# Optimization experiments

Hardware: AMD Instinct MI355X
Metric: run time of the kernel (lower is better)

## Reference

```python
import jax, jax.numpy as jnp
import numpy as np

P = 2          # SamplesLoss p=2
BLUR = 0.05    # eps_final = BLUR**P = 0.0025
SCALING = 0.8  # annealing factor per iteration (on the blur scale)


def _cost(x, y):
    # geomloss cost for p=2: |x - y|^2 / 2, shape (N, M)
    x2 = jnp.sum(x * x, axis=-1)
    y2 = jnp.sum(y * y, axis=-1)
    return 0.5 * (x2[:, None] + y2[None, :] - 2.0 * (x @ y.T))


def _softmin(eps, C, h):
    # -eps * log sum_j exp(h_j - C_ij / eps); h already contains log-weights
    return -eps * jax.nn.logsumexp(h[None, :] - C / eps, axis=1)


def _eps_schedule(x, y):
    # geomloss scaling_parameters / epsilon_schedule with diameter from bounding box
    xn, yn = np.asarray(x), np.asarray(y)
    mins = np.minimum(xn.min(0), yn.min(0))
    maxs = np.maximum(xn.max(0), yn.max(0))
    diameter = float(np.linalg.norm(maxs - mins))
    eps_list = ([diameter ** P]
                + [float(np.exp(e)) for e in np.arange(P * np.log(diameter), P * np.log(BLUR), P * np.log(SCALING))]
                + [BLUR ** P])
    return eps_list


def _sinkhorn_divergence(x, y, eps_list):
    # Debiased Sinkhorn divergence S_eps(x, y), geomloss sinkhorn_tensorized
    N, M = x.shape[0], y.shape[0]
    sg = jax.lax.stop_gradient
    C_xy, C_yx = _cost(x, y), _cost(y, x)
    C_xx, C_yy = _cost(x, sg(x)), _cost(y, sg(y))  # geomloss detaches 2nd arg
    # The annealing loop runs with autograd disabled in geomloss:
    Cxy_, Cyx_, Cxx_, Cyy_ = sg(C_xy), sg(C_yx), sg(C_xx), sg(C_yy)
    a_log = jnp.full((N,), -np.log(N), dtype=x.dtype)  # log uniform weights
    b_log = jnp.full((M,), -np.log(M), dtype=y.dtype)
    e0 = eps_list[0]
    f_aa = _softmin(e0, Cxx_, a_log)
    g_bb = _softmin(e0, Cyy_, b_log)
    g_ab = _softmin(e0, Cyx_, a_log)
    f_ba = _softmin(e0, Cxy_, b_log)
    for eps in eps_list:  # fixed schedule, not a data-dim loop
        ft_ba = _softmin(eps, Cxy_, b_log + g_ab / eps)
        gt_ab = _softmin(eps, Cyx_, a_log + f_ba / eps)
        ft_aa = _softmin(eps, Cxx_, a_log + f_aa / eps)
        gt_bb = _softmin(eps, Cyy_, b_log + g_bb / eps)
        f_ba, g_ab = 0.5 * (f_ba + ft_ba), 0.5 * (g_ab + gt_ab)
        f_aa, g_bb = 0.5 * (f_aa + ft_aa), 0.5 * (g_bb + gt_bb)
    # Final extrapolation step (the only one geomloss differentiates through):
    eps = eps_list[-1]
    f_ba, g_ab = (_softmin(eps, C_xy, sg(b_log + g_ab / eps)),
                  _softmin(eps, C_yx, sg(a_log + f_ba / eps)))
    f_aa = _softmin(eps, C_xx, sg(a_log + f_aa / eps))
    g_bb = _softmin(eps, C_yy, sg(b_log + g_bb / eps))
    # scal with uniform weights == mean
    return jnp.mean(f_ba - f_aa) + jnp.mean(g_ab - g_bb)


def setup_inputs() -> dict:
    key = jax.random.key(0)
    kx, kt = jax.random.split(key)
    x = jax.random.normal(kx, (4096, 64), dtype=jnp.float32)
    target = jax.random.normal(kt, (4096, 64), dtype=jnp.float32)
    return {"x": x, "target": target}


def reference(x, target):
    eps_list = _eps_schedule(x, target)  # concrete schedule from data diameter
    return _sinkhorn_divergence(x, target, eps_list)
```

## Files before the change

### kernel.cpp

```cpp
#include <hip/hip_runtime.h>
#include <math.h>

#define NPTS 4096
#define DIM  64
#define MAX_ITERS 36

#define ALOG (-8.317766166719343f)
#define L2E  (1.4426950408889634f)
#define LN2  (0.6931471805599453f)

#if __has_builtin(__builtin_amdgcn_exp2f)
#define EXP2F(x) __builtin_amdgcn_exp2f(x)
#else
#define EXP2F(x) exp2f(x)
#endif
#if __has_builtin(__builtin_amdgcn_logf)
#define LOG2F(x) __builtin_amdgcn_logf(x)
#else
#define LOG2F(x) log2f(x)
#endif

typedef _Float16 half8 __attribute__((ext_vector_type(8)));

__global__ void minmax_part_kernel(const float* __restrict__ x,
                                   const float* __restrict__ y,
                                   float* __restrict__ partmn,
                                   float* __restrict__ partmx) {
    int t = threadIdx.x;
    int bid = blockIdx.x;
    int g0 = bid * 256 + t;
    const int total = NPTS * DIM;
    float mn = INFINITY, mx = -INFINITY;
    for (int g = g0; g < total; g += 128 * 256) {
        float v = x[g]; mn = fminf(mn, v); mx = fmaxf(mx, v);
        float w = y[g]; mn = fminf(mn, w); mx = fmaxf(mx, w);
    }
    __shared__ float smn[256], smx[256];
    smn[t] = mn; smx[t] = mx;
    __syncthreads();
    if (t < 64) {
        for (int q = 1; q < 4; q++) {
            mn = fminf(mn, smn[t + 64 * q]);
            mx = fmaxf(mx, smx[t + 64 * q]);
        }
        partmn[bid * 64 + t] = mn;
        partmx[bid * 64 + t] = mx;
    }
}

__global__ void schedule_kernel(const float* __restrict__ partmn,
                                const float* __restrict__ partmx,
                                int* __restrict__ hdr,
                                float* __restrict__ sched) {
    int d = threadIdx.x;
    float mn = INFINITY, mx = -INFINITY;
    for (int b = 0; b < 128; b++) {
        mn = fminf(mn, partmn[b * 64 + d]);
        mx = fmaxf(mx, partmx[b * 64 + d]);
    }
    float range = mx - mn;
    __shared__ float r2[64];
    r2[d] = range * range;
    __syncthreads();
    if (d == 0) {
        float ss = 0.f;
        for (int k = 0; k < 64; k++) ss += r2[k];
        float diam_f = sqrtf(ss);
        double diam = (double)diam_f;
        double start = 2.0 * log(diam);
        double stop  = 2.0 * log(0.05);
        double step  = 2.0 * log(0.8);
        int n_ar = (int)ceil((stop - start) / step);
        if (n_ar < 0) n_ar = 0;
        int n_eps = n_ar + 2;
        if (n_eps > 64) n_eps = 64;
        sched[0] = (float)(diam * diam);
        for (int k = 0; k < n_ar && (1 + k) < 63; k++)
            sched[1 + k] = (float)exp(start + step * (double)k);
        sched[n_eps - 1] = 0.0025f;
        for (int k = n_eps; k < 64; k++) sched[k] = 0.0025f;
        hdr[0] = n_eps;
    }
}

__global__ void sqnorm_kernel(const float* __restrict__ X, float* __restrict__ out) {
    int wave = (blockIdx.x * blockDim.x + threadIdx.x) >> 6;
    int lane = threadIdx.x & 63;
    if (wave >= NPTS) return;
    float v = X[wave * DIM + lane];
    float s = v * v;
    for (int o = 32; o > 0; o >>= 1) s += __shfl_xor(s, o, 64);
    if (lane == 0) out[wave] = s;
}

__global__ void hinit_kernel(const float* __restrict__ x2, const float* __restrict__ y2,
                             const float* __restrict__ sched,
                             float* __restrict__ hxy, float* __restrict__ hyx,
                             float* __restrict__ hxx, float* __restrict__ hyy) {
    int j = blockIdx.x * 256 + threadIdx.x;
    float inv20 = L2E / sched[0];
    float b = ALOG * L2E;
    float hx = b - 0.5f * x2[j] * inv20;
    float hy = b - 0.5f * y2[j] * inv20;
    hxy[j] = hy;
    hyx[j] = hx;
    hxx[j] = hx;
    hyy[j] = hy;
}

__global__ __launch_bounds__(256) void gram_kernel(const float* __restrict__ A,
                                                   const float* __restrict__ B,
                                                   _Float16* __restrict__ G) {
    __shared__ float As[64][68], Bs[64][68];
    int t = threadIdx.x;
    int i0 = blockIdx.y * 64, j0 = blockIdx.x * 64;
    for (int q = 0; q < 4; q++) {
        int fi = q * 256 + t;
        int r = fi >> 4, c4 = (fi & 15) * 4;
        *(float4*)&As[r][c4] = *(const float4*)&A[(i0 + r) * DIM + c4];
        *(float4*)&Bs[r][c4] = *(const float4*)&B[(j0 + r) * DIM + c4];
    }
    __syncthreads();
    int tx = t & 15, ty = t >> 4;
    float acc[4][4] = {};
    for (int k4 = 0; k4 < 16; k4++) {
        float4 a4[4], b4[4];
#pragma unroll
        for (int u = 0; u < 4; u++) a4[u] = *(const float4*)&As[ty + 16 * u][k4 * 4];
#pragma unroll
        for (int v = 0; v < 4; v++) b4[v] = *(const float4*)&Bs[tx + 16 * v][k4 * 4];
#pragma unroll
        for (int u = 0; u < 4; u++)
#pragma unroll
            for (int v = 0; v < 4; v++) {
                acc[u][v] = fmaf(a4[u].x, b4[v].x, acc[u][v]);
                acc[u][v] = fmaf(a4[u].y, b4[v].y, acc[u][v]);
                acc[u][v] = fmaf(a4[u].z, b4[v].z, acc[u][v]);
                acc[u][v] = fmaf(a4[u].w, b4[v].w, acc[u][v]);
            }
    }
    for (int u = 0; u < 4; u++)
        for (int v = 0; v < 4; v++)
            G[(size_t)(i0 + ty + 16 * u) * NPTS + j0 + tx + 16 * v] = (_Float16)acc[u][v];
}

struct SMArgs {
    const _Float16* G[4];
    const float* h2in[4];
    float* h2out[4];
    const float* h2cp[4];
    const float* fold[4];
    float* fout[4];
    const float* sqrow[4];
    const int* hdr; const float* sched;
    int t;
};

__global__ __launch_bounds__(256) void softmin_kernel(SMArgs A) {
    int n_eps = A.hdr[0];
    int mat = blockIdx.x >> 10;
    int row = ((blockIdx.x & 1023) << 2) + (threadIdx.x >> 6);
    int lane = threadIdx.x & 63;
    if (A.t >= 0 && A.t >= n_eps) {
        if (lane == 0) {
            A.fout[mat][row] = A.fold[mat][row];
            A.h2out[mat][row] = A.h2cp[mat][row];
        }
        return;
    }
    int idx  = (A.t == -2) ? 0 : ((A.t == -1) ? n_eps - 1 : A.t);
    int nidx = (A.t == -2) ? 0 : ((A.t == -1) ? n_eps - 1 : min(A.t + 1, n_eps - 1));
    float eps = A.sched[idx];
    float inv2 = L2E / eps;
    float inv2n = L2E / A.sched[nidx];
    const _Float16* Gr = A.G[mat] + (size_t)row * NPTS;
    const float* h2v = A.h2in[mat];

    float m = -INFINITY, s = 0.f;
#pragma unroll 2
    for (int c = 0; c < 8; c++) {
        int j0 = c * 512 + lane * 8;
        half8 g8 = *(const half8*)(Gr + j0);
        float4 ha = *(const float4*)(h2v + j0);
        float4 hb = *(const float4*)(h2v + j0 + 4);
        float v0 = fmaf((float)g8[0], inv2, ha.x);
        float v1 = fmaf((float)g8[1], inv2, ha.y);
        float v2 = fmaf((float)g8[2], inv2, ha.z);
        float v3 = fmaf((float)g8[3], inv2, ha.w);
        float v4 = fmaf((float)g8[4], inv2, hb.x);
        float v5 = fmaf((float)g8[5], inv2, hb.y);
        float v6 = fmaf((float)g8[6], inv2, hb.z);
        float v7 = fmaf((float)g8[7], inv2, hb.w);
        float lm = fmaxf(fmaxf(fmaxf(v0, v1), fmaxf(v2, v3)),
                         fmaxf(fmaxf(v4, v5), fmaxf(v6, v7)));
        if (lm > m - 26.0f) {
            float nm = fmaxf(m, lm);
            float acc = s * EXP2F(m - nm);
            acc += EXP2F(v0 - nm) + EXP2F(v1 - nm) + EXP2F(v2 - nm) + EXP2F(v3 - nm);
            acc += EXP2F(v4 - nm) + EXP2F(v5 - nm) + EXP2F(v6 - nm) + EXP2F(v7 - nm);
            m = nm; s = acc;
        }
    }
#pragma unroll
    for (int off = 1; off < 64; off <<= 1) {
        float om = __shfl_xor(m, off, 64);
        float os = __shfl_xor(s, off, 64);
        float nm = fmaxf(m, om);
        s = s * EXP2F(m - nm) + os * EXP2F(om - nm);
        m = nm;
    }
    if (lane == 0) {
        float sq = A.sqrow[mat][row];
        float res = 0.5f * sq - eps * LN2 * (m + LOG2F(s));
        float fnew = (A.t >= 0) ? 0.5f * (A.fold[mat][row] + res) : res;
        A.fout[mat][row] = fnew;
        A.h2out[mat][row] = ALOG * L2E + (fnew - 0.5f * sq) * inv2n;
    }
}

__global__ void reduce_kernel(const float* __restrict__ fba, const float* __restrict__ faa,
                              const float* __restrict__ gab, const float* __restrict__ gbb,
                              float* __restrict__ out) {
    int t = threadIdx.x;
    double s1 = 0.0, s2 = 0.0;
    for (int i = t; i < NPTS; i += 256) {
        s1 += (double)fba[i] - (double)faa[i];
        s2 += (double)gab[i] - (double)gbb[i];
    }
    __shared__ double sh1[256], sh2[256];
    sh1[t] = s1; sh2[t] = s2;
    __syncthreads();
    for (int o = 128; o > 0; o >>= 1) {
        if (t < o) { sh1[t] += sh1[t + o]; sh2[t] += sh2[t + o]; }
        __syncthreads();
    }
    if (t == 0) out[0] = (float)(sh1[0] / NPTS + sh2[0] / NPTS);
}

extern "C" void kernel_launch(void* const* d_in, const int* in_sizes, int n_in,
                              void* d_out, int out_size, void* d_ws, size_t ws_size,
                              hipStream_t stream) {
    const float* x = (const float*)d_in[0];
    const float* y = (const float*)d_in[1];
    float* out = (float*)d_out;
    float* w = (float*)d_ws;

    int*   hdr   = (int*)w;
    float* sched = w + 16;
    float* pmn   = w + 80;
    float* pmx   = w + 8272;
    float* x2    = w + 16464;
    float* y2    = w + 20560;
    float* fb = w + 24656;
    float* hb = w + 57424;
    auto F  = [&](int mat, int p) { return fb + (mat * 2 + p) * 4096; };
    auto H2 = [&](int mat, int p) { return hb + (mat * 2 + p) * 4096; };
    const size_t NN = (size_t)NPTS * NPTS;
    _Float16* Gm[4];
    Gm[0] = (_Float16*)(w + 98304);
    Gm[1] = Gm[0] + NN;
    Gm[2] = Gm[1] + NN;
    Gm[3] = Gm[2] + NN;
    const int couple[4] = {1, 0, 2, 3};

    hipLaunchKernelGGL(minmax_part_kernel, dim3(128), dim3(256), 0, stream, x, y, pmn, pmx);
    hipLaunchKernelGGL(schedule_kernel, dim3(1), dim3(64), 0, stream, pmn, pmx, hdr, sched);
    hipLaunchKernelGGL(sqnorm_kernel, dim3(1024), dim3(256), 0, stream, x, x2);
    hipLaunchKernelGGL(sqnorm_kernel, dim3(1024), dim3(256), 0, stream, y, y2);
    hipLaunchKernelGGL(gram_kernel, dim3(64, 64), dim3(256), 0, stream, x, y, Gm[0]);
    hipLaunchKernelGGL(gram_kernel, dim3(64, 64), dim3(256), 0, stream, y, x, Gm[1]);
    hipLaunchKernelGGL(gram_kernel, dim3(64, 64), dim3(256), 0, stream, x, x, Gm[2]);
    hipLaunchKernelGGL(gram_kernel, dim3(64, 64), dim3(256), 0, stream, y, y, Gm[3]);
    hipLaunchKernelGGL(hinit_kernel, dim3(16), dim3(256), 0, stream,
                       x2, y2, sched, H2(0, 0), H2(1, 0), H2(2, 0), H2(3, 0));

    SMArgs SA;
    for (int m = 0; m < 4; m++) SA.G[m] = Gm[m];
    SA.sqrow[0] = x2; SA.sqrow[1] = y2; SA.sqrow[2] = x2; SA.sqrow[3] = y2;
    SA.hdr = hdr; SA.sched = sched;

    for (int m = 0; m < 4; m++) {
        SA.h2in[m] = H2(m, 0);
        SA.h2out[m] = H2(couple[m], 1);
        SA.h2cp[m] = H2(couple[m], 0);
        SA.fold[m] = F(m, 1);
        SA.fout[m] = F(m, 0);
    }
    SA.t = -2;
    hipLaunchKernelGGL(softmin_kernel, dim3(4096), dim3(256), 0, stream, SA);

    for (int t = 0; t < MAX_ITERS; t++) {
        int pf = t & 1;
        for (int m = 0; m < 4; m++) {
            SA.h2in[m] = H2(m, 1 - pf);
            SA.h2out[m] = H2(couple[m], pf);
            SA.h2cp[m] = H2(couple[m], 1 - pf);
            SA.fold[m] = F(m, pf);
            SA.fout[m] = F(m, 1 - pf);
        }
        SA.t = t;
        hipLaunchKernelGGL(softmin_kernel, dim3(4096), dim3(256), 0, stream, SA);
    }

    for (int m = 0; m < 4; m++) {
        SA.h2in[m] = H2(m, 1);
        SA.h2out[m] = H2(couple[m], 0);
        SA.h2cp[m] = H2(couple[m], 1);
        SA.fold[m] = F(m, 0);
        SA.fout[m] = F(m, 1);
    }
    SA.t = -1;
    hipLaunchKernelGGL(softmin_kernel, dim3(4096), dim3(256), 0, stream, SA);

    hipLaunchKernelGGL(reduce_kernel, dim3(1), dim3(256), 0, stream,
                       F(0, 1), F(2, 1), F(1, 1), F(3, 1), out);
}
```

Baseline: 1.076 ms.

## Recompute Gram tiles with MFMA each pass instead of streaming stored fp16 matrices

The four precomputed 4096x4096 fp16 Gram matrices are dropped. Each softmin pass now recomputes the dot products on the fly with 16x16x32 f16 MFMA instructions from fp16 copies of the inputs, so the per-iteration 128MB memory stream becomes compute. Column work is split into four chunks whose partial max and sum are merged by a new small combine kernel. This doubles the launch count and adds a partial-result round trip through memory, in exchange for removing the bandwidth-bound matrix reads.

```diff
diff --git a/kernel.cpp b/kernel.cpp
--- a/kernel.cpp
+++ b/kernel.cpp
@@ -20,7 +20,8 @@
 #define LOG2F(x) log2f(x)
 #endif
 
-typedef _Float16 half8 __attribute__((ext_vector_type(8)));
+typedef _Float16 f16x8 __attribute__((ext_vector_type(8)));
+typedef float    f32x4 __attribute__((ext_vector_type(4)));
 
 __global__ void minmax_part_kernel(const float* __restrict__ x,
                                    const float* __restrict__ y,
@@ -93,6 +94,13 @@
     if (lane == 0) out[wave] = s;
 }
 
+__global__ void cast_kernel(const float* __restrict__ x, const float* __restrict__ y,
+                            _Float16* __restrict__ X16, _Float16* __restrict__ Y16) {
+    int g = blockIdx.x * 256 + threadIdx.x;
+    X16[g] = (_Float16)x[g];
+    Y16[g] = (_Float16)y[g];
+}
+
 __global__ void hinit_kernel(const float* __restrict__ x2, const float* __restrict__ y2,
                              const float* __restrict__ sched,
                              float* __restrict__ hxy, float* __restrict__ hyx,
@@ -108,114 +116,126 @@
     hyy[j] = hy;
 }
 
-__global__ __launch_bounds__(256) void gram_kernel(const float* __restrict__ A,
-                                                   const float* __restrict__ B,
-                                                   _Float16* __restrict__ G) {
-    __shared__ float As[64][68], Bs[64][68];
-    int t = threadIdx.x;
-    int i0 = blockIdx.y * 64, j0 = blockIdx.x * 64;
-    for (int q = 0; q < 4; q++) {
-        int fi = q * 256 + t;
-        int r = fi >> 4, c4 = (fi & 15) * 4;
-        *(float4*)&As[r][c4] = *(const float4*)&A[(i0 + r) * DIM + c4];
-        *(float4*)&Bs[r][c4] = *(const float4*)&B[(j0 + r) * DIM + c4];
-    }
-    __syncthreads();
-    int tx = t & 15, ty = t >> 4;
-    float acc[4][4] = {};
-    for (int k4 = 0; k4 < 16; k4++) {
-        float4 a4[4], b4[4];
-#pragma unroll
-        for (int u = 0; u < 4; u++) a4[u] = *(const float4*)&As[ty + 16 * u][k4 * 4];
-#pragma unroll
-        for (int v = 0; v < 4; v++) b4[v] = *(const float4*)&Bs[tx + 16 * v][k4 * 4];
-#pragma unroll
-        for (int u = 0; u < 4; u++)
-#pragma unroll
-            for (int v = 0; v < 4; v++) {
-                acc[u][v] = fmaf(a4[u].x, b4[v].x, acc[u][v]);
-                acc[u][v] = fmaf(a4[u].y, b4[v].y, acc[u][v]);
-                acc[u][v] = fmaf(a4[u].z, b4[v].z, acc[u][v]);
-                acc[u][v] = fmaf(a4[u].w, b4[v].w, acc[u][v]);
-            }
-    }
-    for (int u = 0; u < 4; u++)
-        for (int v = 0; v < 4; v++)
-            G[(size_t)(i0 + ty + 16 * u) * NPTS + j0 + tx + 16 * v] = (_Float16)acc[u][v];
-}
-
-struct SMArgs {
-    const _Float16* G[4];
+struct PassArgs {
+    const _Float16* Am[4];
+    const _Float16* Bm[4];
     const float* h2in[4];
-    float* h2out[4];
-    const float* h2cp[4];
-    const float* fold[4];
-    float* fout[4];
-    const float* sqrow[4];
+    float* Pm; float* Ps;
     const int* hdr; const float* sched;
     int t;
 };
 
-__global__ __launch_bounds__(256) void softmin_kernel(SMArgs A) {
+__global__ __launch_bounds__(256) void pass_kernel(PassArgs A) {
     int n_eps = A.hdr[0];
-    int mat = blockIdx.x >> 10;
-    int row = ((blockIdx.x & 1023) << 2) + (threadIdx.x >> 6);
-    int lane = threadIdx.x & 63;
+    if (A.t >= 0 && A.t >= n_eps) return;
+    int idx = (A.t == -2) ? 0 : ((A.t == -1) ? n_eps - 1 : A.t);
+    float inv2 = L2E / A.sched[idx];
+
+    int b = blockIdx.x;
+    int mat = b >> 8, rb = (b >> 2) & 63, cs = b & 3;
+    const _Float16* Amat = A.Am[mat];
+    const _Float16* Bmat = A.Bm[mat] + (size_t)(cs * 1024) * DIM;
+    const float* h2v = A.h2in[mat] + cs * 1024;
+
+    __shared__ float hs[1024];
+    int tt = threadIdx.x;
+    *(float4*)&hs[tt * 4] = *(const float4*)&h2v[tt * 4];
+    __syncthreads();
+
+    int wave = tt >> 6, lane = tt & 63;
+    int quad = lane >> 4, lo = lane & 15;
+    int row0 = rb * 64 + wave * 16;
+
+    const _Float16* arow = Amat + (size_t)(row0 + lo) * DIM + quad * 8;
+    f16x8 a0 = *(const f16x8*)(arow);
+    f16x8 a1 = *(const f16x8*)(arow + 32);
+
+    float m[4] = {-INFINITY, -INFINITY, -INFINITY, -INFINITY};
+    float s[4] = {0.f, 0.f, 0.f, 0.f};
+
+    for (int sb = 0; sb < 16; sb++) {
+        float v[4][4];
+#pragma unroll
+        for (int cc = 0; cc < 4; cc++) {
+            int cb = sb * 64 + cc * 16;
+            const _Float16* brow = Bmat + (size_t)(cb + lo) * DIM + quad * 8;
+            f16x8 b0 = *(const f16x8*)(brow);
+            f16x8 b1 = *(const f16x8*)(brow + 32);
+            f32x4 acc = {0.f, 0.f, 0.f, 0.f};
+            acc = __builtin_amdgcn_mfma_f32_16x16x32_f16(a0, b0, acc, 0, 0, 0);
+            acc = __builtin_amdgcn_mfma_f32_16x16x32_f16(a1, b1, acc, 0, 0, 0);
+            float hval = hs[cb + lo];
+#pragma unroll
+            for (int r = 0; r < 4; r++) v[r][cc] = fmaf(acc[r], inv2, hval);
+        }
+#pragma unroll
+        for (int r = 0; r < 4; r++) {
+            float lm = fmaxf(fmaxf(v[r][0], v[r][1]), fmaxf(v[r][2], v[r][3]));
+            if (lm > m[r] - 26.0f) {
+                float nm = fmaxf(m[r], lm);
+                float acc = s[r] * EXP2F(m[r] - nm);
+                acc += EXP2F(v[r][0] - nm) + EXP2F(v[r][1] - nm)
+                     + EXP2F(v[r][2] - nm) + EXP2F(v[r][3] - nm);
+                m[r] = nm; s[r] = acc;
+            }
+        }
+    }
+#pragma unroll
+    for (int off = 1; off < 16; off <<= 1) {
+#pragma unroll
+        for (int r = 0; r < 4; r++) {
+            float om = __shfl_xor(m[r], off, 64);
+            float os = __shfl_xor(s[r], off, 64);
+            float nm = fmaxf(m[r], om);
+            s[r] = s[r] * EXP2F(m[r] - nm) + os * EXP2F(om - nm);
+            m[r] = nm;
+        }
+    }
+    if (lo == 0) {
+#pragma unroll
+        for (int r = 0; r < 4; r++) {
+            int row = row0 + quad * 4 + r;
+            int pi = (mat * 4 + cs) * NPTS + row;
+            A.Pm[pi] = m[r]; A.Ps[pi] = s[r];
+        }
+    }
+}
+
+struct CombArgs {
+    const float* Pm; const float* Ps;
+    const float* sq[4];
+    const float* fold[4]; float* fout[4];
+    float* h2out[4];
+    const float* h2cp[4];
+    const int* hdr; const float* sched;
+    int t;
+};
+
+__global__ void comb_kernel(CombArgs A) {
+    int g = blockIdx.x * 256 + threadIdx.x;
+    int mat = g >> 12, row = g & 4095;
+    int n_eps = A.hdr[0];
     if (A.t >= 0 && A.t >= n_eps) {
-        if (lane == 0) {
-            A.fout[mat][row] = A.fold[mat][row];
-            A.h2out[mat][row] = A.h2cp[mat][row];
-        }
+        A.fout[mat][row] = A.fold[mat][row];
+        A.h2out[mat][row] = A.h2cp[mat][row];
         return;
     }
     int idx  = (A.t == -2) ? 0 : ((A.t == -1) ? n_eps - 1 : A.t);
     int nidx = (A.t == -2) ? 0 : ((A.t == -1) ? n_eps - 1 : min(A.t + 1, n_eps - 1));
     float eps = A.sched[idx];
-    float inv2 = L2E / eps;
     float inv2n = L2E / A.sched[nidx];
-    const _Float16* Gr = A.G[mat] + (size_t)row * NPTS;
-    const float* h2v = A.h2in[mat];
-
-    float m = -INFINITY, s = 0.f;
-#pragma unroll 2
-    for (int c = 0; c < 8; c++) {
-        int j0 = c * 512 + lane * 8;
-        half8 g8 = *(const half8*)(Gr + j0);
-        float4 ha = *(const float4*)(h2v + j0);
-        float4 hb = *(const float4*)(h2v + j0 + 4);
-        float v0 = fmaf((float)g8[0], inv2, ha.x);
-        float v1 = fmaf((float)g8[1], inv2, ha.y);
-        float v2 = fmaf((float)g8[2], inv2, ha.z);
-        float v3 = fmaf((float)g8[3], inv2, ha.w);
-        float v4 = fmaf((float)g8[4], inv2, hb.x);
-        float v5 = fmaf((float)g8[5], inv2, hb.y);
-        float v6 = fmaf((float)g8[6], inv2, hb.z);
-        float v7 = fmaf((float)g8[7], inv2, hb.w);
-        float lm = fmaxf(fmaxf(fmaxf(v0, v1), fmaxf(v2, v3)),
-                         fmaxf(fmaxf(v4, v5), fmaxf(v6, v7)));
-        if (lm > m - 26.0f) {
-            float nm = fmaxf(m, lm);
-            float acc = s * EXP2F(m - nm);
-            acc += EXP2F(v0 - nm) + EXP2F(v1 - nm) + EXP2F(v2 - nm) + EXP2F(v3 - nm);
-            acc += EXP2F(v4 - nm) + EXP2F(v5 - nm) + EXP2F(v6 - nm) + EXP2F(v7 - nm);
-            m = nm; s = acc;
-        }
-    }
-#pragma unroll
-    for (int off = 1; off < 64; off <<= 1) {
-        float om = __shfl_xor(m, off, 64);
-        float os = __shfl_xor(s, off, 64);
-        float nm = fmaxf(m, om);
-        s = s * EXP2F(m - nm) + os * EXP2F(om - nm);
-        m = nm;
-    }
-    if (lane == 0) {
-        float sq = A.sqrow[mat][row];
-        float res = 0.5f * sq - eps * LN2 * (m + LOG2F(s));
-        float fnew = (A.t >= 0) ? 0.5f * (A.fold[mat][row] + res) : res;
-        A.fout[mat][row] = fnew;
-        A.h2out[mat][row] = ALOG * L2E + (fnew - 0.5f * sq) * inv2n;
-    }
+    float M = -INFINITY;
+#pragma unroll
+    for (int q = 0; q < 4; q++) M = fmaxf(M, A.Pm[(mat * 4 + q) * NPTS + row]);
+    float S = 0.f;
+#pragma unroll
+    for (int q = 0; q < 4; q++)
+        S += A.Ps[(mat * 4 + q) * NPTS + row] * EXP2F(A.Pm[(mat * 4 + q) * NPTS + row] - M);
+    float sq = A.sq[mat][row];
+    float res = 0.5f * sq - eps * LN2 * (M + LOG2F(S));
+    float fnew = (A.t >= 0) ? 0.5f * (A.fold[mat][row] + res) : res;
+    A.fout[mat][row] = fnew;
+    A.h2out[mat][row] = ALOG * L2E + (fnew - 0.5f * sq) * inv2n;
 }
 
 __global__ void reduce_kernel(const float* __restrict__ fba, const float* __restrict__ faa,
@@ -251,66 +271,68 @@
     float* pmx   = w + 8272;
     float* x2    = w + 16464;
     float* y2    = w + 20560;
-    float* fb = w + 24656;
-    float* hb = w + 57424;
+    float* fb    = w + 24656;
+    float* hb    = w + 57424;
     auto F  = [&](int mat, int p) { return fb + (mat * 2 + p) * 4096; };
     auto H2 = [&](int mat, int p) { return hb + (mat * 2 + p) * 4096; };
-    const size_t NN = (size_t)NPTS * NPTS;
-    _Float16* Gm[4];
-    Gm[0] = (_Float16*)(w + 98304);
-    Gm[1] = Gm[0] + NN;
-    Gm[2] = Gm[1] + NN;
-    Gm[3] = Gm[2] + NN;
+    float* Pm = w + 90192;
+    float* Ps = w + 155728;
+    _Float16* X16 = (_Float16*)(w + 221264);
+    _Float16* Y16 = (_Float16*)(w + 352336);
     const int couple[4] = {1, 0, 2, 3};
 
     hipLaunchKernelGGL(minmax_part_kernel, dim3(128), dim3(256), 0, stream, x, y, pmn, pmx);
     hipLaunchKernelGGL(schedule_kernel, dim3(1), dim3(64), 0, stream, pmn, pmx, hdr, sched);
     hipLaunchKernelGGL(sqnorm_kernel, dim3(1024), dim3(256), 0, stream, x, x2);
     hipLaunchKernelGGL(sqnorm_kernel, dim3(1024), dim3(256), 0, stream, y, y2);
-    hipLaunchKernelGGL(gram_kernel, dim3(64, 64), dim3(256), 0, stream, x, y, Gm[0]);
-    hipLaunchKernelGGL(gram_kernel, dim3(64, 64), dim3(256), 0, stream, y, x, Gm[1]);
-    hipLaunchKernelGGL(gram_kernel, dim3(64, 64), dim3(256), 0, stream, x, x, Gm[2]);
-    hipLaunchKernelGGL(gram_kernel, dim3(64, 64), dim3(256), 0, stream, y, y, Gm[3]);
+    hipLaunchKernelGGL(cast_kernel, dim3(1024), dim3(256), 0, stream, x, y, X16, Y16);
     hipLaunchKernelGGL(hinit_kernel, dim3(16), dim3(256), 0, stream,
                        x2, y2, sched, H2(0, 0), H2(1, 0), H2(2, 0), H2(3, 0));
 
-    SMArgs SA;
-    for (int m = 0; m < 4; m++) SA.G[m] = Gm[m];
-    SA.sqrow[0] = x2; SA.sqrow[1] = y2; SA.sqrow[2] = x2; SA.sqrow[3] = y2;
-    SA.hdr = hdr; SA.sched = sched;
-
+    PassArgs PA;
+    PA.Am[0] = X16; PA.Bm[0] = Y16;
+    PA.Am[1] = Y16; PA.Bm[1] = X16;
+    PA.Am[2] = X16; PA.Bm[2] = X16;
+    PA.Am[3] = Y16; PA.Bm[3] = Y16;
+    PA.Pm = Pm; PA.Ps = Ps; PA.hdr = hdr; PA.sched = sched;
+
+    CombArgs CA;
+    CA.Pm = Pm; CA.Ps = Ps;
+    CA.sq[0] = x2; CA.sq[1] = y2; CA.sq[2] = x2; CA.sq[3] = y2;
+    CA.hdr = hdr; CA.sched = sched;
+
+    for (int m = 0; m < 4; m++) PA.h2in[m] = H2(m, 0);
+    PA.t = -2;
+    hipLaunchKernelGGL(pass_kernel, dim3(1024), dim3(256), 0, stream, PA);
     for (int m = 0; m < 4; m++) {
-        SA.h2in[m] = H2(m, 0);
-        SA.h2out[m] = H2(couple[m], 1);
-        SA.h2cp[m] = H2(couple[m], 0);
-        SA.fold[m] = F(m, 1);
-        SA.fout[m] = F(m, 0);
-    }
-    SA.t = -2;
-    hipLaunchKernelGGL(softmin_kernel, dim3(4096), dim3(256), 0, stream, SA);
+        CA.fold[m] = F(m, 1); CA.fout[m] = F(m, 0);
+        CA.h2out[m] = H2(couple[m], 1); CA.h2cp[m] = H2(couple[m], 0);
+    }
+    CA.t = -2;
+    hipLaunchKernelGGL(comb_kernel, dim3(64), dim3(256), 0, stream, CA);
 
     for (int t = 0; t < MAX_ITERS; t++) {
         int pf = t & 1;
+        for (int m = 0; m < 4; m++) PA.h2in[m] = H2(m, 1 - pf);
+        PA.t = t;
+        hipLaunchKernelGGL(pass_kernel, dim3(1024), dim3(256), 0, stream, PA);
         for (int m = 0; m < 4; m++) {
-            SA.h2in[m] = H2(m, 1 - pf);
-            SA.h2out[m] = H2(couple[m], pf);
-            SA.h2cp[m] = H2(couple[m], 1 - pf);
-            SA.fold[m] = F(m, pf);
-            SA.fout[m] = F(m, 1 - pf);
-        }
-        SA.t = t;
-        hipLaunchKernelGGL(softmin_kernel, dim3(4096), dim3(256), 0, stream, SA);
-    }
-
+            CA.fold[m] = F(m, pf); CA.fout[m] = F(m, 1 - pf);
+            CA.h2out[m] = H2(couple[m], pf); CA.h2cp[m] = H2(couple[m], 1 - pf);
+        }
+        CA.t = t;
+        hipLaunchKernelGGL(comb_kernel, dim3(64), dim3(256), 0, stream, CA);
+    }
+
+    for (int m = 0; m < 4; m++) PA.h2in[m] = H2(m, 1);
+    PA.t = -1;
+    hipLaunchKernelGGL(pass_kernel, dim3(1024), dim3(256), 0, stream, PA);
     for (int m = 0; m < 4; m++) {
-        SA.h2in[m] = H2(m, 1);
-        SA.h2out[m] = H2(couple[m], 0);
-        SA.h2cp[m] = H2(couple[m], 1);
-        SA.fold[m] = F(m, 0);
-        SA.fout[m] = F(m, 1);
-    }
-    SA.t = -1;
-    hipLaunchKernelGGL(softmin_kernel, dim3(4096), dim3(256), 0, stream, SA);
+        CA.fold[m] = F(m, 0); CA.fout[m] = F(m, 1);
+        CA.h2out[m] = H2(couple[m], 0); CA.h2cp[m] = H2(couple[m], 1);
+    }
+    CA.t = -1;
+    hipLaunchKernelGGL(comb_kernel, dim3(64), dim3(256), 0, stream, CA);
 
     hipLaunchKernelGGL(reduce_kernel, dim3(1), dim3(256), 0, stream,
                        F(0, 1), F(2, 1), F(1, 1), F(3, 1), out);
```

Measured after the change: 2.350 ms. 2.18x slower.
